# Kernel tuning notes

Hardware: AMD Instinct MI355X
Metric: run time of the kernel (lower is better)

Reference implementation:

```python
import jax, jax.numpy as jnp
import numpy as np

ALPHA = 0.7
N = 4194304
NUM_ACTIONS = 3


def setup_inputs() -> dict:
    key = jax.random.key(0)
    k1, k2, k3, k4, k5 = jax.random.split(key, 5)
    return {
        "pred_prices": jax.random.normal(k1, (N,), dtype=jnp.float32),
        "pred_actions": jax.random.normal(k2, (N, NUM_ACTIONS), dtype=jnp.float32),
        "tgt_prices": jax.random.normal(k3, (N,), dtype=jnp.float32),
        "tgt_actions": jax.random.randint(k4, (N,), 0, NUM_ACTIONS, dtype=jnp.int64),
        "prices": jax.random.normal(k5, (N,), dtype=jnp.float32),
    }


def reference(pred_prices, pred_actions, tgt_prices, tgt_actions, prices):
    # MSE over price predictions
    price_loss = jnp.mean((pred_prices - tgt_prices) ** 2)

    # Cross-entropy (mean over batch), matches nn.CrossEntropyLoss on logits
    logp = jax.nn.log_softmax(pred_actions, axis=-1)  # [N, 3]
    action_loss = -jnp.mean(jnp.take_along_axis(logp, tgt_actions[:, None], axis=-1))

    # Vectorized replacement of the per-sample profit loop (no_grad in original)
    predicted_actions = jnp.argmax(pred_actions, axis=-1)  # [N]
    p = tgt_prices
    d = p[1:] - p[:-1]                     # [N-1]
    zero = jnp.zeros((1,), p.dtype)
    diff_fwd = jnp.concatenate([d, zero])  # p[i+1]-p[i], last entry 0
    diff_bwd = jnp.concatenate([zero, d])  # p[i]-p[i-1], first entry 0
    profits = jnp.where(predicted_actions == 0, diff_fwd,
                        jnp.where(predicted_actions == 2, diff_bwd,
                                  jnp.zeros_like(p)))
    profit_weight = jax.nn.sigmoid(profits * 10.0)
    weighted_action_loss = action_loss * jnp.mean(profit_weight)

    return ALPHA * weighted_action_loss + (1.0 - ALPHA) * price_loss
```

## Files before the change

### kernel.cpp

```cpp
#include <hip/hip_runtime.h>

static constexpr int NN  = 4194304;
static constexpr int NB  = 4096;
static constexpr int TPB = 256;

__global__ __launch_bounds__(256) void pfl_main(
    const float* __restrict__ pp,
    const float* __restrict__ pa,
    const float* __restrict__ tp,
    const int*   __restrict__ ta,
    float* __restrict__ bsum)
{
    const int tid = threadIdx.x;
    const int bid = blockIdx.x;
    const int g   = bid * TPB + tid;
    const int i   = g * 4;

    const float4* pp4 = (const float4*)pp;
    const float4* tp4 = (const float4*)tp;
    const float4* pa4 = (const float4*)pa;
    const int4*   ta4 = (const int4*)ta;

    float4 p  = pp4[g];
    float4 t  = tp4[g];
    int4   a  = ta4[g];
    float4 A0 = pa4[3*g + 0];
    float4 A1 = pa4[3*g + 1];
    float4 A2 = pa4[3*g + 2];
    float tm1 = (i > 0)      ? tp[i - 1] : 0.f;
    float tnx = (i + 4 < NN) ? tp[i + 4] : 0.f;

    float tv[6] = {tm1, t.x, t.y, t.z, t.w, tnx};
    float pv[4] = {p.x, p.y, p.z, p.w};
    float rows[4][3] = {{A0.x, A0.y, A0.z},
                        {A0.w, A1.x, A1.y},
                        {A1.z, A1.w, A2.x},
                        {A2.y, A2.z, A2.w}};
    int av[4] = {a.x, a.y, a.z, a.w};

    float sq = 0.f, ce = 0.f, pw = 0.f;

    #pragma unroll
    for (int j = 0; j < 4; ++j) {
        const int idx = i + j;
        float d = pv[j] - tv[j + 1];
        sq += d * d;

        float x0 = rows[j][0], x1 = rows[j][1], x2 = rows[j][2];
        float m  = fmaxf(x0, fmaxf(x1, x2));
        float lse = m + __logf(__expf(x0 - m) + __expf(x1 - m) + __expf(x2 - m));
        float tgt = (av[j] == 0) ? x0 : ((av[j] == 1) ? x1 : x2);
        ce += lse - tgt;

        int pidx = 0;
        float best = x0;
        if (x1 > best) { best = x1; pidx = 1; }
        if (x2 > best) { pidx = 2; }

        float profit = 0.f;
        if (pidx == 0)      profit = (idx + 1 < NN) ? (tv[j + 2] - tv[j + 1]) : 0.f;
        else if (pidx == 2) profit = (idx > 0)      ? (tv[j + 1] - tv[j])     : 0.f;

        pw += 1.f / (1.f + __expf(-10.f * profit));
    }

    #pragma unroll
    for (int off = 32; off > 0; off >>= 1) {
        sq += __shfl_down(sq, off, 64);
        ce += __shfl_down(ce, off, 64);
        pw += __shfl_down(pw, off, 64);
    }

    __shared__ float s_sq[4], s_ce[4], s_pw[4];
    const int lane = tid & 63;
    const int wid  = tid >> 6;
    if (lane == 0) { s_sq[wid] = sq; s_ce[wid] = ce; s_pw[wid] = pw; }
    __syncthreads();

    if (tid == 0) {
        bsum[bid]          = s_sq[0] + s_sq[1] + s_sq[2] + s_sq[3];
        bsum[NB + bid]     = s_ce[0] + s_ce[1] + s_ce[2] + s_ce[3];
        bsum[2 * NB + bid] = s_pw[0] + s_pw[1] + s_pw[2] + s_pw[3];
    }
}

__global__ __launch_bounds__(1024) void pfl_final(const float* __restrict__ bsum,
                                                  float* __restrict__ out) {
    const int tid = threadIdx.x;
    const float4* b4 = (const float4*)bsum;
    const int Q = NB / 4;

    float4 vsq = b4[tid];
    float4 vce = b4[Q + tid];
    float4 vpw = b4[2 * Q + tid];

    double sq = (double)vsq.x + vsq.y + vsq.z + vsq.w;
    double ce = (double)vce.x + vce.y + vce.z + vce.w;
    double pw = (double)vpw.x + vpw.y + vpw.z + vpw.w;

    #pragma unroll
    for (int off = 32; off > 0; off >>= 1) {
        sq += __shfl_down(sq, off, 64);
        ce += __shfl_down(ce, off, 64);
        pw += __shfl_down(pw, off, 64);
    }

    __shared__ double s_sq[16], s_ce[16], s_pw[16];
    const int lane = tid & 63;
    const int wid  = tid >> 6;
    if (lane == 0) { s_sq[wid] = sq; s_ce[wid] = ce; s_pw[wid] = pw; }
    __syncthreads();

    if (tid == 0) {
        double tsq = 0.0, tce = 0.0, tpw = 0.0;
        #pragma unroll
        for (int w = 0; w < 16; ++w) { tsq += s_sq[w]; tce += s_ce[w]; tpw += s_pw[w]; }
        const double inv = 1.0 / (double)NN;
        out[0] = (float)(0.7 * (tce * inv) * (tpw * inv) + 0.3 * (tsq * inv));
    }
}

extern "C" void kernel_launch(void* const* d_in, const int* in_sizes, int n_in,
                              void* d_out, int out_size, void* d_ws, size_t ws_size,
                              hipStream_t stream) {
    const float* pp = (const float*)d_in[0];
    const float* pa = (const float*)d_in[1];
    const float* tp = (const float*)d_in[2];
    const int*   ta = (const int*)d_in[3];

    float* bsum = (float*)d_ws;

    pfl_main<<<NB, TPB, 0, stream>>>(pp, pa, tp, ta, bsum);
    pfl_final<<<1, 1024, 0, stream>>>(bsum, (float*)d_out);
}
```

Before: 133.6 us.

## Coalesce action-logit loads via LDS transpose and shuffle neighbor prices

Action logits are now read as contiguous float4 chunks across the block (tid, tid+256, tid+512) and redistributed through a padded shared-memory buffer, so each thread still gets its 12 values. The old pattern had each thread read three consecutive float4s with a stride of 48 bytes. Neighboring target prices come from wavefront shuffles, and only lanes 0 and 63 issue the extra scalar global loads. This adds an LDS round-trip and a block barrier before compute, and 13 KB of shared memory per block, which may reduce occupancy.

```diff
diff --git a/kernel.cpp b/kernel.cpp
--- a/kernel.cpp
+++ b/kernel.cpp
@@ -18,25 +18,45 @@
 
     const float4* pp4 = (const float4*)pp;
     const float4* tp4 = (const float4*)tp;
-    const float4* pa4 = (const float4*)pa;
     const int4*   ta4 = (const int4*)ta;
+    const float4* paB = (const float4*)pa + (size_t)bid * (TPB * 3);
 
+    float4 f0 = paB[tid];
+    float4 f1 = paB[tid + TPB];
+    float4 f2 = paB[tid + 2 * TPB];
     float4 p  = pp4[g];
     float4 t  = tp4[g];
     int4   a  = ta4[g];
-    float4 A0 = pa4[3*g + 0];
-    float4 A1 = pa4[3*g + 1];
-    float4 A2 = pa4[3*g + 2];
-    float tm1 = (i > 0)      ? tp[i - 1] : 0.f;
-    float tnx = (i + 4 < NN) ? tp[i + 4] : 0.f;
+
+    const int lane = tid & 63;
+    float tm1 = __shfl_up(t.w, 1, 64);
+    float tnx = __shfl_down(t.x, 1, 64);
+    if (lane == 0)  tm1 = (i > 0)      ? tp[i - 1] : 0.f;
+    if (lane == 63) tnx = (i + 4 < NN) ? tp[i + 4] : 0.f;
+
+    __shared__ float lds[TPB * 13];
+    {
+        float v[12] = {f0.x, f0.y, f0.z, f0.w,
+                       f1.x, f1.y, f1.z, f1.w,
+                       f2.x, f2.y, f2.z, f2.w};
+        #pragma unroll
+        for (int c = 0; c < 12; ++c) {
+            int q = ((c >> 2) == 0 ? 0 : ((c >> 2) == 1 ? 1024 : 2048)) + 4 * tid + (c & 3);
+            lds[13 * (q / 12) + (q % 12)] = v[c];
+        }
+    }
+    __syncthreads();
+
+    float rows[4][3];
+    #pragma unroll
+    for (int j = 0; j < 4; ++j)
+        #pragma unroll
+        for (int c = 0; c < 3; ++c)
+            rows[j][c] = lds[13 * tid + 3 * j + c];
 
     float tv[6] = {tm1, t.x, t.y, t.z, t.w, tnx};
     float pv[4] = {p.x, p.y, p.z, p.w};
-    float rows[4][3] = {{A0.x, A0.y, A0.z},
-                        {A0.w, A1.x, A1.y},
-                        {A1.z, A1.w, A2.x},
-                        {A2.y, A2.z, A2.w}};
-    int av[4] = {a.x, a.y, a.z, a.w};
+    int   av[4] = {a.x, a.y, a.z, a.w};
 
     float sq = 0.f, ce = 0.f, pw = 0.f;
 
@@ -72,8 +92,7 @@
     }
 
     __shared__ float s_sq[4], s_ce[4], s_pw[4];
-    const int lane = tid & 63;
-    const int wid  = tid >> 6;
+    const int wid = tid >> 6;
     if (lane == 0) { s_sq[wid] = sq; s_ce[wid] = ce; s_pw[wid] = pw; }
     __syncthreads();
 
```

Result: slower. 138.3 us (+3.5%).
